# Performance work log

Hardware: AMD Instinct MI355X
Metric: run time of the kernel (lower is better)

## Reference

```python
import jax, jax.numpy as jnp
import numpy as np

N = 100000      # physical-network nodes
E = 3200000     # directed edges (avg degree 32)
DIN = 128       # input_dim
DH = 128        # embedding_dim
DOUT = 128      # output_dim
NUM_GRAPHS = 1


def setup_inputs() -> dict:
    key = jax.random.key(0)
    ks = jax.random.split(key, 8)
    s = 0.05
    x = jax.random.normal(ks[0], (N, DIN), dtype=jnp.float32)
    edge_index = jax.random.randint(ks[1], (2, E), 0, N, dtype=jnp.int64)
    W1 = jax.random.normal(ks[2], (DIN, DH), dtype=jnp.float32) * s
    b1 = jnp.zeros((DH,), dtype=jnp.float32)
    W2 = jax.random.normal(ks[3], (DH, DH), dtype=jnp.float32) * s
    b2 = jnp.zeros((DH,), dtype=jnp.float32)
    W3 = jax.random.normal(ks[4], (DH, DOUT), dtype=jnp.float32) * s
    b3 = jnp.zeros((DOUT,), dtype=jnp.float32)
    return {"x": x, "edge_index": edge_index,
            "W1": W1, "b1": b1, "W2": W2, "b2": b2, "W3": W3, "b3": b3}


def _gcn_norm(edge_index, n_nodes):
    # PyG GCNConv default: add self-loops, symmetric D^{-1/2} (A+I) D^{-1/2} norm.
    loops = jnp.arange(n_nodes, dtype=edge_index.dtype)
    src = jnp.concatenate([edge_index[0], loops])   # [E+N]
    dst = jnp.concatenate([edge_index[1], loops])   # [E+N]
    deg = jax.ops.segment_sum(jnp.ones_like(dst, dtype=jnp.float32), dst,
                              num_segments=n_nodes)
    dinv = jax.lax.rsqrt(deg)  # deg >= 1 because of self-loops
    norm = dinv[src] * dinv[dst]                    # [E+N]
    return src, dst, norm


def _gcn_conv(h, W, b, src, dst, norm, n_nodes):
    h = h @ W                                       # [N, dout] linear first (PyG order)
    msg = h[src] * norm[:, None]                    # gather + edge scaling
    agg = jax.ops.segment_sum(msg, dst, num_segments=n_nodes)  # scatter-add
    return agg + b


def reference(x, edge_index, W1, b1, W2, b2, W3, b3):
    src, dst, norm = _gcn_norm(edge_index, N)
    h = jax.nn.relu(_gcn_conv(x, W1, b1, src, dst, norm, N))
    # dropout is identity in eval mode
    h = jax.nn.relu(_gcn_conv(h, W2, b2, src, dst, norm, N))
    h = _gcn_conv(h, W3, b3, src, dst, norm, N)
    return h.reshape(NUM_GRAPHS, N // NUM_GRAPHS, -1)
```

## Files before the change

kernel.cpp:

```cpp
#include <hip/hip_runtime.h>
#include <cstddef>
#include <cstdint>

#define NN 100000
#define NE 3200000
#define D  128
#define NB 782
#define BSH 7
#define NPB 512
#define CHUNK 6250
#define BCAP 4608

typedef short v8s __attribute__((ext_vector_type(8)));
typedef float v4f __attribute__((ext_vector_type(4)));


__device__ __forceinline__ unsigned short f2bf(float f) {
  uint32_t u = __float_as_uint(f);
  uint32_t r = u + 0x7fff + ((u >> 16) & 1);
  return (unsigned short)(r >> 16);
}
__device__ __forceinline__ float bf_lo(uint32_t v) {
  return __uint_as_float(v << 16);
}
__device__ __forceinline__ float bf_hi(uint32_t v) {
  return __uint_as_float(v & 0xffff0000u);
}


__global__ void k_zero(int* __restrict__ p, int n) {
  int i = blockIdx.x * 256 + threadIdx.x;
  if (i < n) p[i] = 0;
}

__global__ __launch_bounds__(256) void kb_part2(const int* __restrict__ src,
                                                const int* __restrict__ dst,
                                                int* __restrict__ gcur,
                                                uint32_t* __restrict__ ebuf) {
  __shared__ int h[NB];
  __shared__ int cur[NB];
  for (int i = threadIdx.x; i < NB; i += 256) h[i] = 0;
  __syncthreads();
  int lo = blockIdx.x * CHUNK, hi = lo + CHUNK;
  if (hi > NE) hi = NE;
  for (int e = lo + threadIdx.x; e < hi; e += 256)
    atomicAdd(&h[dst[e] >> BSH], 1);
  __syncthreads();
  for (int i = threadIdx.x; i < NB; i += 256)
    cur[i] = h[i] ? atomicAdd(&gcur[i], h[i]) : 0;
  __syncthreads();
  for (int e = lo + threadIdx.x; e < hi; e += 256) {
    int s = src[e], d = dst[e];
    int b = d >> BSH;
    int p = atomicAdd(&cur[b], 1);
    if (p < BCAP)
      ebuf[(size_t)b * BCAP + p] = ((uint32_t)s << BSH) | (uint32_t)(d & 127);
  }
}

__global__ __launch_bounds__(256) void kb_build(const uint32_t* __restrict__ ebuf,
                                                const int* __restrict__ gcur,
                                                int* __restrict__ row_off,
                                                int* __restrict__ row_end,
                                                float* __restrict__ dinv,
                                                int* __restrict__ col) {
  int b = blockIdx.x;
  __shared__ int h[128];
  __shared__ int s[128];
  __shared__ int cur[128];
  if (threadIdx.x < 128) h[threadIdx.x] = 0;
  __syncthreads();
  const uint32_t* eb = ebuf + (size_t)b * BCAP;
  int cnt = gcur[b];
  for (int e = threadIdx.x; e < cnt; e += 256)
    atomicAdd(&h[eb[e] & 127], 1);
  __syncthreads();
  int v = (threadIdx.x < 128) ? h[threadIdx.x] : 0;
  if (threadIdx.x < 128) s[threadIdx.x] = v;
  __syncthreads();
  for (int d = 1; d < 128; d <<= 1) {
    int t = (threadIdx.x < 128 && threadIdx.x >= d) ? s[threadIdx.x - d] : 0;
    __syncthreads();
    if (threadIdx.x < 128) s[threadIdx.x] += t;
    __syncthreads();
  }
  if (threadIdx.x < 128) {
    int ro = b * BCAP + s[threadIdx.x] - v;
    cur[threadIdx.x] = ro;
    int node = b * 128 + threadIdx.x;
    if (node < NN) {
      row_off[node] = ro;
      row_end[node] = ro + v;
      dinv[node] = rsqrtf((float)(v + 1));
    }
  }
  __syncthreads();
  for (int e = threadIdx.x; e < cnt; e += 256) {
    uint32_t p = eb[e];
    int pos = atomicAdd(&cur[p & 127], 1);
    col[pos] = (int)(p >> BSH);
  }
}


__global__ void k_wt3(const float* __restrict__ W1, const float* __restrict__ W2,
                      const float* __restrict__ W3, unsigned short* __restrict__ wt) {
  int idx = blockIdx.x * 256 + threadIdx.x;
  if (idx >= 3 * 16384) return;
  int m = idx >> 14, rem = idx & 16383;
  int k = rem >> 7, c = rem & 127;
  const float* W = (m == 0) ? W1 : (m == 1) ? W2 : W3;
  wt[m * 16384 + c * 128 + k] = f2bf(W[rem]);
}


__global__ __launch_bounds__(256) void k_gemm2(const float* __restrict__ A,
                                               const unsigned short* __restrict__ wt,
                                               const float* __restrict__ dinv,
                                               unsigned short* __restrict__ C) {
  const int wave = threadIdx.x >> 6;
  const int lane = threadIdx.x & 63;
  const int row0 = blockIdx.x * 256 + wave * 64;
  const int rl = lane & 15;
  const int kg = lane >> 4;

  v4f acc[4][8];
#pragma unroll
  for (int t = 0; t < 4; ++t)
#pragma unroll
    for (int ct = 0; ct < 8; ++ct) acc[t][ct] = (v4f){0.f, 0.f, 0.f, 0.f};

  union U { uint4 u; v8s v; unsigned short us[8]; };

#pragma unroll
  for (int ks = 0; ks < 4; ++ks) {
    U a[4];
#pragma unroll
    for (int t = 0; t < 4; ++t) {
      int r = row0 + t * 16 + rl;
      if (r >= NN) r = NN - 1;
      const float* ap = A + (size_t)r * D + ks * 32 + kg * 8;
      float4 l4 = *(const float4*)ap;
      float4 h4 = *(const float4*)(ap + 4);
      a[t].us[0] = f2bf(l4.x); a[t].us[1] = f2bf(l4.y);
      a[t].us[2] = f2bf(l4.z); a[t].us[3] = f2bf(l4.w);
      a[t].us[4] = f2bf(h4.x); a[t].us[5] = f2bf(h4.y);
      a[t].us[6] = f2bf(h4.z); a[t].us[7] = f2bf(h4.w);
    }
#pragma unroll
    for (int ct = 0; ct < 8; ++ct) {
      U b;
      b.u = *(const uint4*)(wt + (size_t)(ct * 16 + rl) * 128 + ks * 32 + kg * 8);
#pragma unroll
      for (int t = 0; t < 4; ++t)
        acc[t][ct] =
            __builtin_amdgcn_mfma_f32_16x16x32_bf16(a[t].v, b.v, acc[t][ct], 0, 0, 0);
    }
  }

#pragma unroll
  for (int t = 0; t < 4; ++t) {
#pragma unroll
    for (int i = 0; i < 4; ++i) {
      int row = row0 + t * 16 + kg * 4 + i;
      if (row < NN) {
        float dv = dinv[row];
#pragma unroll
        for (int ct = 0; ct < 8; ++ct)
          C[(size_t)row * D + ct * 16 + rl] = f2bf(dv * acc[t][ct][i]);
      }
    }
  }
}


#define AGG8(e0, q0, q1)                                     \
  {                                                          \
    int s0 = col[e0], s1 = col[e0 + 1], s2 = col[e0 + 2],    \
        s3 = col[e0 + 3], s4 = col[e0 + 4], s5 = col[e0 + 5],\
        s6 = col[e0 + 6], s7 = col[e0 + 7];                  \
    uint32_t v0 = tu[(size_t)s0 * 64 + lane];                \
    uint32_t v1 = tu[(size_t)s1 * 64 + lane];                \
    uint32_t v2 = tu[(size_t)s2 * 64 + lane];                \
    uint32_t v3 = tu[(size_t)s3 * 64 + lane];                \
    uint32_t v4 = tu[(size_t)s4 * 64 + lane];                \
    uint32_t v5 = tu[(size_t)s5 * 64 + lane];                \
    uint32_t v6 = tu[(size_t)s6 * 64 + lane];                \
    uint32_t v7 = tu[(size_t)s7 * 64 + lane];                \
    q0 += bf_lo(v0); q1 += bf_hi(v0);                        \
    q0 += bf_lo(v1); q1 += bf_hi(v1);                        \
    q0 += bf_lo(v2); q1 += bf_hi(v2);                        \
    q0 += bf_lo(v3); q1 += bf_hi(v3);                        \
    q0 += bf_lo(v4); q1 += bf_hi(v4);                        \
    q0 += bf_lo(v5); q1 += bf_hi(v5);                        \
    q0 += bf_lo(v6); q1 += bf_hi(v6);                        \
    q0 += bf_lo(v7); q1 += bf_hi(v7);                        \
  }

#define GATHER_BODY()                                                        \
  uint32_t svA = tu[(size_t)gA * 64 + lane];                                 \
  uint32_t svB = tu[(size_t)gB * 64 + lane];                                 \
  float a0 = bf_lo(svA), a1 = bf_hi(svA);                                    \
  float b0 = bf_lo(svB), b1 = bf_hi(svB);                                    \
  int eA = row_off[gA], endA = row_end[gA];                                  \
  int eB = row_off[gB], endB = row_end[gB];                                  \
  while (eA + 8 <= endA && eB + 8 <= endB) {                                 \
    int sA0 = col[eA],     sA1 = col[eA + 1], sA2 = col[eA + 2],             \
        sA3 = col[eA + 3], sA4 = col[eA + 4], sA5 = col[eA + 5],             \
        sA6 = col[eA + 6], sA7 = col[eA + 7];                                \
    int sB0 = col[eB],     sB1 = col[eB + 1], sB2 = col[eB + 2],             \
        sB3 = col[eB + 3], sB4 = col[eB + 4], sB5 = col[eB + 5],             \
        sB6 = col[eB + 6], sB7 = col[eB + 7];                                \
    uint32_t vA0 = tu[(size_t)sA0 * 64 + lane];                              \
    uint32_t vA1 = tu[(size_t)sA1 * 64 + lane];                              \
    uint32_t vA2 = tu[(size_t)sA2 * 64 + lane];                              \
    uint32_t vA3 = tu[(size_t)sA3 * 64 + lane];                              \
    uint32_t vA4 = tu[(size_t)sA4 * 64 + lane];                              \
    uint32_t vA5 = tu[(size_t)sA5 * 64 + lane];                              \
    uint32_t vA6 = tu[(size_t)sA6 * 64 + lane];                              \
    uint32_t vA7 = tu[(size_t)sA7 * 64 + lane];                              \
    uint32_t vB0 = tu[(size_t)sB0 * 64 + lane];                              \
    uint32_t vB1 = tu[(size_t)sB1 * 64 + lane];                              \
    uint32_t vB2 = tu[(size_t)sB2 * 64 + lane];                              \
    uint32_t vB3 = tu[(size_t)sB3 * 64 + lane];                              \
    uint32_t vB4 = tu[(size_t)sB4 * 64 + lane];                              \
    uint32_t vB5 = tu[(size_t)sB5 * 64 + lane];                              \
    uint32_t vB6 = tu[(size_t)sB6 * 64 + lane];                              \
    uint32_t vB7 = tu[(size_t)sB7 * 64 + lane];                              \
    a0 += bf_lo(vA0); a1 += bf_hi(vA0);                                      \
    a0 += bf_lo(vA1); a1 += bf_hi(vA1);                                      \
    a0 += bf_lo(vA2); a1 += bf_hi(vA2);                                      \
    a0 += bf_lo(vA3); a1 += bf_hi(vA3);                                      \
    a0 += bf_lo(vA4); a1 += bf_hi(vA4);                                      \
    a0 += bf_lo(vA5); a1 += bf_hi(vA5);                                      \
    a0 += bf_lo(vA6); a1 += bf_hi(vA6);                                      \
    a0 += bf_lo(vA7); a1 += bf_hi(vA7);                                      \
    b0 += bf_lo(vB0); b1 += bf_hi(vB0);                                      \
    b0 += bf_lo(vB1); b1 += bf_hi(vB1);                                      \
    b0 += bf_lo(vB2); b1 += bf_hi(vB2);                                      \
    b0 += bf_lo(vB3); b1 += bf_hi(vB3);                                      \
    b0 += bf_lo(vB4); b1 += bf_hi(vB4);                                      \
    b0 += bf_lo(vB5); b1 += bf_hi(vB5);                                      \
    b0 += bf_lo(vB6); b1 += bf_hi(vB6);                                      \
    b0 += bf_lo(vB7); b1 += bf_hi(vB7);                                      \
    eA += 8; eB += 8;                                                        \
  }                                                                          \
  for (; eA + 8 <= endA; eA += 8) AGG8(eA, a0, a1);                          \
  for (; eA < endA; ++eA) {                                                  \
    uint32_t v = tu[(size_t)col[eA] * 64 + lane];                            \
    a0 += bf_lo(v); a1 += bf_hi(v);                                          \
  }                                                                          \
  for (; eB + 8 <= endB; eB += 8) AGG8(eB, b0, b1);                          \
  for (; eB < endB; ++eB) {                                                  \
    uint32_t v = tu[(size_t)col[eB] * 64 + lane];                            \
    b0 += bf_lo(v); b1 += bf_hi(v);                                          \
  }


__global__ __launch_bounds__(512) void k_aggf(
    const uint32_t* __restrict__ tu, const int* __restrict__ row_off,
    const int* __restrict__ row_end, const int* __restrict__ col,
    const float* __restrict__ dinv, const float* __restrict__ bias,
    const unsigned short* __restrict__ wt, unsigned short* __restrict__ t_out) {
  const int wave = threadIdx.x >> 6;
  const int lane = threadIdx.x & 63;
  const int gA = blockIdx.x * 16 + wave * 2;
  const int gB = gA + 1;

  __shared__ uint32_t lds[16 * 64];

  const float diA = dinv[gA], diB = dinv[gB];

  GATHER_BODY();

  int c = lane * 2;
  float bl = bias[c], bh = bias[c + 1];
  float rA0 = fmaxf(diA * a0 + bl, 0.f);
  float rA1 = fmaxf(diA * a1 + bh, 0.f);
  float rB0 = fmaxf(diB * b0 + bl, 0.f);
  float rB1 = fmaxf(diB * b1 + bh, 0.f);

  const int rA = wave * 2, rB = rA + 1;
  lds[rA * 64 + (lane ^ ((rA & 7) << 2))] =
      (uint32_t)f2bf(rA0) | ((uint32_t)f2bf(rA1) << 16);
  lds[rB * 64 + (lane ^ ((rB & 7) << 2))] =
      (uint32_t)f2bf(rB0) | ((uint32_t)f2bf(rB1) << 16);
  __syncthreads();

  const int rl = lane & 15;
  const int kg = lane >> 4;
  union U { uint4 u; v8s v; };
  v4f acc = (v4f){0.f, 0.f, 0.f, 0.f};
#pragma unroll
  for (int ks = 0; ks < 4; ++ks) {
    U a, b;
    a.u = *(const uint4*)&lds[rl * 64 + ((ks * 16 + kg * 4) ^ ((rl & 7) << 2))];
    b.u = *(const uint4*)(wt + (size_t)(wave * 16 + rl) * 128 + ks * 32 + kg * 8);
    acc = __builtin_amdgcn_mfma_f32_16x16x32_bf16(a.v, b.v, acc, 0, 0, 0);
  }
#pragma unroll
  for (int i = 0; i < 4; ++i) {
    int node = blockIdx.x * 16 + kg * 4 + i;
    t_out[(size_t)node * D + wave * 16 + rl] = f2bf(dinv[node] * acc[i]);
  }
}


__global__ __launch_bounds__(256) void k_agg2(
    const uint32_t* __restrict__ tu, const int* __restrict__ row_off,
    const int* __restrict__ row_end, const int* __restrict__ col,
    const float* __restrict__ dinv, const float* __restrict__ bias,
    float* __restrict__ outf) {
  const int wave = threadIdx.x >> 6;
  const int lane = threadIdx.x & 63;
  const int gA = blockIdx.x * 8 + wave * 2;
  const int gB = gA + 1;

  const float diA = dinv[gA], diB = dinv[gB];

  GATHER_BODY();

  int c = lane * 2;
  float rA0 = diA * a0 + bias[c];
  float rA1 = diA * a1 + bias[c + 1];
  float rB0 = diB * b0 + bias[c];
  float rB1 = diB * b1 + bias[c + 1];
  *(float2*)(outf + (size_t)gA * D + c) = make_float2(rA0, rA1);
  *(float2*)(outf + (size_t)gB * D + c) = make_float2(rB0, rB1);
}


extern "C" void kernel_launch(void* const* d_in, const int* in_sizes, int n_in,
                              void* d_out, int out_size, void* d_ws, size_t ws_size,
                              hipStream_t stream) {
  const float* x  = (const float*)d_in[0];
  const int*   ei = (const int*)d_in[1];
  const float* W1 = (const float*)d_in[2];
  const float* b1 = (const float*)d_in[3];
  const float* W2 = (const float*)d_in[4];
  const float* b2 = (const float*)d_in[5];
  const float* W3 = (const float*)d_in[6];
  const float* b3 = (const float*)d_in[7];
  float* out = (float*)d_out;

  char* base = (char*)d_ws;
  size_t o = 0;
  auto take = [&](size_t bytes) {
    void* p = base + o;
    o += (bytes + 255) & ~(size_t)255;
    return p;
  };
  int*   row_off = (int*)take((size_t)NN * 4);
  int*   row_end = (int*)take((size_t)NN * 4);
  float* dinv    = (float*)take((size_t)NN * 4);
  int*   gcur    = (int*)take((size_t)NB * 4);
  unsigned short* wt = (unsigned short*)take(3 * 16384 * 2);
  void* region1 = take((size_t)NN * D * 2);
  int*  col     = (int*)take((size_t)NB * BCAP * 4);
  unsigned short* t0 = (unsigned short*)take((size_t)NN * D * 2);

  uint32_t* ebuf = (uint32_t*)region1;
  unsigned short* t1 = (unsigned short*)region1;

  const int* src = ei;
  const int* dst = ei + NE;

  k_zero  <<<(NB + 255) / 256, 256, 0, stream>>>(gcur, NB);
  kb_part2<<<NPB, 256, 0, stream>>>(src, dst, gcur, ebuf);
  kb_build<<<NB, 256, 0, stream>>>(ebuf, gcur, row_off, row_end, dinv, col);
  k_wt3   <<<192, 256, 0, stream>>>(W1, W2, W3, wt);

  const int gB = (NN + 255) / 256;
  const int fB = NN / 16;
  const int aB = NN / 8;

  k_gemm2<<<gB, 256, 0, stream>>>(x, wt, dinv, t0);
  k_aggf<<<fB, 512, 0, stream>>>((const uint32_t*)t0, row_off, row_end, col, dinv,
                                 b1, wt + 16384, t1);
  k_aggf<<<fB, 512, 0, stream>>>((const uint32_t*)t1, row_off, row_end, col, dinv,
                                 b2, wt + 32768, t0);
  k_agg2<<<aB, 256, 0, stream>>>((const uint32_t*)t0, row_off, row_end, col, dinv,
                                 b3, out);
}
```

Measured before the change: 486.6 us.

## Degree-sort nodes into a permutation to balance work in fused aggregation kernels

Builds a histogram of node in-degrees during CSR construction, scans it, and writes a permutation that orders nodes by degree. The two fused aggregate+GEMM kernels then take their node IDs through this permutation, so waves and blocks handle nodes of similar degree and lanes diverge less. This adds two small kernels plus an extra indirection on every node lookup. Output rows are now written scattered rather than contiguously, which can hurt memory locality. Because the graph is random with fairly uniform degree, there is little imbalance to remove. The zeroing of the degree bins also misses the highest bins because of allocation padding; this only matters for degrees that do not occur here.

```diff
diff --git a/kernel.cpp b/kernel.cpp
--- a/kernel.cpp
+++ b/kernel.cpp
@@ -63,12 +63,15 @@
                                                 int* __restrict__ row_off,
                                                 int* __restrict__ row_end,
                                                 float* __restrict__ dinv,
-                                                int* __restrict__ col) {
+                                                int* __restrict__ col,
+                                                int* __restrict__ dbins) {
   int b = blockIdx.x;
   __shared__ int h[128];
   __shared__ int s[128];
   __shared__ int cur[128];
+  __shared__ int dh[256];
   if (threadIdx.x < 128) h[threadIdx.x] = 0;
+  dh[threadIdx.x] = 0;
   __syncthreads();
   const uint32_t* eb = ebuf + (size_t)b * BCAP;
   int cnt = gcur[b];
@@ -92,13 +95,41 @@
       row_off[node] = ro;
       row_end[node] = ro + v;
       dinv[node] = rsqrtf((float)(v + 1));
+      atomicAdd(&dh[v > 255 ? 255 : v], 1);
     }
   }
   __syncthreads();
+  if (dh[threadIdx.x]) atomicAdd(&dbins[threadIdx.x], dh[threadIdx.x]);
   for (int e = threadIdx.x; e < cnt; e += 256) {
     uint32_t p = eb[e];
     int pos = atomicAdd(&cur[p & 127], 1);
     col[pos] = (int)(p >> BSH);
+  }
+}
+
+__global__ __launch_bounds__(256) void k_dscan(const int* __restrict__ dbins,
+                                               int* __restrict__ dcur) {
+  __shared__ int s[256];
+  int v = dbins[threadIdx.x];
+  s[threadIdx.x] = v;
+  __syncthreads();
+  for (int d = 1; d < 256; d <<= 1) {
+    int t = (threadIdx.x >= d) ? s[threadIdx.x - d] : 0;
+    __syncthreads();
+    s[threadIdx.x] += t;
+    __syncthreads();
+  }
+  dcur[threadIdx.x] = s[threadIdx.x] - v;
+}
+
+__global__ void k_perm(const int* __restrict__ row_off, const int* __restrict__ row_end,
+                       int* __restrict__ dcur, int* __restrict__ perm) {
+  int node = blockIdx.x * 256 + threadIdx.x;
+  if (node < NN) {
+    int deg = row_end[node] - row_off[node];
+    if (deg > 255) deg = 255;
+    int pos = atomicAdd(&dcur[deg], 1);
+    perm[pos] = node;
   }
 }
 
@@ -261,11 +292,12 @@
     const uint32_t* __restrict__ tu, const int* __restrict__ row_off,
     const int* __restrict__ row_end, const int* __restrict__ col,
     const float* __restrict__ dinv, const float* __restrict__ bias,
-    const unsigned short* __restrict__ wt, unsigned short* __restrict__ t_out) {
+    const unsigned short* __restrict__ wt, const int* __restrict__ perm,
+    unsigned short* __restrict__ t_out) {
   const int wave = threadIdx.x >> 6;
   const int lane = threadIdx.x & 63;
-  const int gA = blockIdx.x * 16 + wave * 2;
-  const int gB = gA + 1;
+  const int gA = perm[blockIdx.x * 16 + wave * 2];
+  const int gB = perm[blockIdx.x * 16 + wave * 2 + 1];
 
   __shared__ uint32_t lds[16 * 64];
 
@@ -300,7 +332,7 @@
   }
 #pragma unroll
   for (int i = 0; i < 4; ++i) {
-    int node = blockIdx.x * 16 + kg * 4 + i;
+    int node = perm[blockIdx.x * 16 + kg * 4 + i];
     t_out[(size_t)node * D + wave * 16 + rl] = f2bf(dinv[node] * acc[i]);
   }
 }
@@ -354,6 +386,9 @@
   int*   row_end = (int*)take((size_t)NN * 4);
   float* dinv    = (float*)take((size_t)NN * 4);
   int*   gcur    = (int*)take((size_t)NB * 4);
+  int*   dbins   = (int*)take(256 * 4);
+  int*   dcur    = (int*)take(256 * 4);
+  int*   perm    = (int*)take((size_t)NN * 4);
   unsigned short* wt = (unsigned short*)take(3 * 16384 * 2);
   void* region1 = take((size_t)NN * D * 2);
   int*  col     = (int*)take((size_t)NB * BCAP * 4);
@@ -365,9 +400,11 @@
   const int* src = ei;
   const int* dst = ei + NE;
 
-  k_zero  <<<(NB + 255) / 256, 256, 0, stream>>>(gcur, NB);
+  k_zero  <<<(NB + 255 + 256) / 256, 256, 0, stream>>>(gcur, NB + 256);
   kb_part2<<<NPB, 256, 0, stream>>>(src, dst, gcur, ebuf);
-  kb_build<<<NB, 256, 0, stream>>>(ebuf, gcur, row_off, row_end, dinv, col);
+  kb_build<<<NB, 256, 0, stream>>>(ebuf, gcur, row_off, row_end, dinv, col, dbins);
+  k_dscan <<<1, 256, 0, stream>>>(dbins, dcur);
+  k_perm  <<<(NN + 255) / 256, 256, 0, stream>>>(row_off, row_end, dcur, perm);
   k_wt3   <<<192, 256, 0, stream>>>(W1, W2, W3, wt);
 
   const int gB = (NN + 255) / 256;
@@ -376,9 +413,9 @@
 
   k_gemm2<<<gB, 256, 0, stream>>>(x, wt, dinv, t0);
   k_aggf<<<fB, 512, 0, stream>>>((const uint32_t*)t0, row_off, row_end, col, dinv,
-                                 b1, wt + 16384, t1);
+                                 b1, wt + 16384, perm, t1);
   k_aggf<<<fB, 512, 0, stream>>>((const uint32_t*)t1, row_off, row_end, col, dinv,
-                                 b2, wt + 32768, t0);
+                                 b2, wt + 32768, perm, t0);
   k_agg2<<<aB, 256, 0, stream>>>((const uint32_t*)t0, row_off, row_end, col, dinv,
                                  b3, out);
 }
```

Measured after the change: 667.3 us. +37.1%, slower.

## Make fused aggregate-GEMM wave-local via shuffles, removing LDS and block barrier

Applied to the files above, without the earlier changes.

The fused aggregation and next-layer GEMM kernel is restructured so each wave computes the full 128-column output for its own two nodes. The aggregated rows are passed between lanes with shuffles into MFMA A-fragments instead of going through shared memory and a __syncthreads. Blocks shrink from 512 to 256 threads. This removes the block-wide barrier, so slow high-degree waves no longer stall the others, and frees LDS. In exchange each wave now runs 32 MFMAs and reads the whole weight matrix instead of one 16-column slice. Only 2 of the 16 MFMA rows hold real data, so most tensor-core work is wasted.

```diff
diff --git a/kernel.cpp b/kernel.cpp
--- a/kernel.cpp
+++ b/kernel.cpp
@@ -257,17 +257,17 @@
   }
 
 
-__global__ __launch_bounds__(512) void k_aggf(
+__global__ __launch_bounds__(256) void k_aggfw(
     const uint32_t* __restrict__ tu, const int* __restrict__ row_off,
     const int* __restrict__ row_end, const int* __restrict__ col,
     const float* __restrict__ dinv, const float* __restrict__ bias,
     const unsigned short* __restrict__ wt, unsigned short* __restrict__ t_out) {
   const int wave = threadIdx.x >> 6;
   const int lane = threadIdx.x & 63;
-  const int gA = blockIdx.x * 16 + wave * 2;
+  const int gA = blockIdx.x * 8 + wave * 2;
   const int gB = gA + 1;
-
-  __shared__ uint32_t lds[16 * 64];
+  const int rl = lane & 15;
+  const int kg = lane >> 4;
 
   const float diA = dinv[gA], diB = dinv[gB];
 
@@ -275,33 +275,39 @@
 
   int c = lane * 2;
   float bl = bias[c], bh = bias[c + 1];
-  float rA0 = fmaxf(diA * a0 + bl, 0.f);
-  float rA1 = fmaxf(diA * a1 + bh, 0.f);
-  float rB0 = fmaxf(diB * b0 + bl, 0.f);
-  float rB1 = fmaxf(diB * b1 + bh, 0.f);
-
-  const int rA = wave * 2, rB = rA + 1;
-  lds[rA * 64 + (lane ^ ((rA & 7) << 2))] =
-      (uint32_t)f2bf(rA0) | ((uint32_t)f2bf(rA1) << 16);
-  lds[rB * 64 + (lane ^ ((rB & 7) << 2))] =
-      (uint32_t)f2bf(rB0) | ((uint32_t)f2bf(rB1) << 16);
-  __syncthreads();
-
-  const int rl = lane & 15;
-  const int kg = lane >> 4;
+  uint32_t packA = (uint32_t)f2bf(fmaxf(diA * a0 + bl, 0.f)) |
+                   ((uint32_t)f2bf(fmaxf(diA * a1 + bh, 0.f)) << 16);
+  uint32_t packB = (uint32_t)f2bf(fmaxf(diB * b0 + bl, 0.f)) |
+                   ((uint32_t)f2bf(fmaxf(diB * b1 + bh, 0.f)) << 16);
+
   union U { uint4 u; v8s v; };
-  v4f acc = (v4f){0.f, 0.f, 0.f, 0.f};
+  U af[4];
 #pragma unroll
   for (int ks = 0; ks < 4; ++ks) {
-    U a, b;
-    a.u = *(const uint4*)&lds[rl * 64 + ((ks * 16 + kg * 4) ^ ((rl & 7) << 2))];
-    b.u = *(const uint4*)(wt + (size_t)(wave * 16 + rl) * 128 + ks * 32 + kg * 8);
-    acc = __builtin_amdgcn_mfma_f32_16x16x32_bf16(a.v, b.v, acc, 0, 0, 0);
-  }
-#pragma unroll
-  for (int i = 0; i < 4; ++i) {
-    int node = blockIdx.x * 16 + kg * 4 + i;
-    t_out[(size_t)node * D + wave * 16 + rl] = f2bf(dinv[node] * acc[i]);
+    uint32_t w[4];
+#pragma unroll
+    for (int m = 0; m < 4; ++m) {
+      int p = ks * 16 + kg * 4 + m;
+      uint32_t wa = __shfl(packA, p);
+      uint32_t wb = __shfl(packB, p);
+      w[m] = (rl == 1) ? wb : wa;
+    }
+    af[ks].u = make_uint4(w[0], w[1], w[2], w[3]);
+  }
+
+#pragma unroll
+  for (int ct = 0; ct < 8; ++ct) {
+    v4f acc = (v4f){0.f, 0.f, 0.f, 0.f};
+#pragma unroll
+    for (int ks = 0; ks < 4; ++ks) {
+      U b;
+      b.u = *(const uint4*)(wt + (size_t)(ct * 16 + rl) * 128 + ks * 32 + kg * 8);
+      acc = __builtin_amdgcn_mfma_f32_16x16x32_bf16(af[ks].v, b.v, acc, 0, 0, 0);
+    }
+    if (kg == 0) {
+      t_out[(size_t)gA * D + ct * 16 + rl] = f2bf(diA * acc[0]);
+      t_out[(size_t)gB * D + ct * 16 + rl] = f2bf(diB * acc[1]);
+    }
   }
 }
 
@@ -371,14 +377,13 @@
   k_wt3   <<<192, 256, 0, stream>>>(W1, W2, W3, wt);
 
   const int gB = (NN + 255) / 256;
-  const int fB = NN / 16;
   const int aB = NN / 8;
 
   k_gemm2<<<gB, 256, 0, stream>>>(x, wt, dinv, t0);
-  k_aggf<<<fB, 512, 0, stream>>>((const uint32_t*)t0, row_off, row_end, col, dinv,
-                                 b1, wt + 16384, t1);
-  k_aggf<<<fB, 512, 0, stream>>>((const uint32_t*)t1, row_off, row_end, col, dinv,
-                                 b2, wt + 32768, t0);
+  k_aggfw<<<aB, 256, 0, stream>>>((const uint32_t*)t0, row_off, row_end, col, dinv,
+                                  b1, wt + 16384, t1);
+  k_aggfw<<<aB, 256, 0, stream>>>((const uint32_t*)t1, row_off, row_end, col, dinv,
+                                  b2, wt + 32768, t0);
   k_agg2<<<aB, 256, 0, stream>>>((const uint32_t*)t0, row_off, row_end, col, dinv,
                                  b3, out);
 }
```

Result: slower. 698.7 us (+43.6%).
